# Optimization experiments

Measured on AMD Instinct MI355X. Metric: run time of the kernel, lower is better.

Reference implementation:

```python
import jax, jax.numpy as jnp
import numpy as np

D = 128      # feature dim
H = 8        # heads
DH = D // H  # dim per head
N = 100000   # nodes
E = 600000   # edges
BN_EPS = 1e-5


def _bn(x, g, b, m, v):
    # BatchNorm1d in eval mode (running stats)
    return (x - m) * jax.lax.rsqrt(v + BN_EPS) * g + b


def setup_inputs() -> dict:
    key = jax.random.key(0)
    ks = jax.random.split(key, 32)
    s = 1.0 / np.sqrt(D)
    inp = {
        "x": jax.random.normal(ks[0], (N, D), jnp.float32),
        "edge_index": jax.random.randint(ks[1], (2, E), 0, N, jnp.int64),
        # type embeddings (1 node type, 1 edge type)
        "nt_emb": jax.random.normal(ks[2], (1, D), jnp.float32),
        "et_emb": jax.random.normal(ks[3], (1, D), jnp.float32),
        # merge_node_edge_attr: Linear(2D,D) -> BN -> ReLU -> Linear(D,D)
        "mW1": jax.random.normal(ks[4], (2 * D, D), jnp.float32) * s,
        "mb1": jnp.zeros((D,), jnp.float32),
        "m_g": jnp.ones((D,), jnp.float32),
        "m_b": jnp.zeros((D,), jnp.float32),
        "m_m": jax.random.normal(ks[5], (D,), jnp.float32) * 0.1,
        "m_v": jax.random.uniform(ks[6], (D,), jnp.float32, 0.5, 1.5),
        "mW2": jax.random.normal(ks[7], (D, D), jnp.float32) * s,
        "mb2": jnp.zeros((D,), jnp.float32),
        # residual projection (no bias)
        "resW": jax.random.normal(ks[8], (D, D), jnp.float32) * s,
        # attention projections
        "qW": jax.random.normal(ks[9], (D, D), jnp.float32) * s,
        "qb": jnp.zeros((D,), jnp.float32),
        "kW": jax.random.normal(ks[10], (D, D), jnp.float32) * s,
        "kb": jnp.zeros((D,), jnp.float32),
        "vW": jax.random.normal(ks[11], (D, D), jnp.float32) * s,
        "vb": jnp.zeros((D,), jnp.float32),
        # output mlp: Linear -> BN -> LeakyReLU -> Linear
        "oW1": jax.random.normal(ks[12], (D, D), jnp.float32) * s,
        "ob1": jnp.zeros((D,), jnp.float32),
        "o_g": jnp.ones((D,), jnp.float32),
        "o_b": jnp.zeros((D,), jnp.float32),
        "o_m": jax.random.normal(ks[13], (D,), jnp.float32) * 0.1,
        "o_v": jax.random.uniform(ks[14], (D,), jnp.float32, 0.5, 1.5),
        "oW2": jax.random.normal(ks[15], (D, D), jnp.float32) * s,
        "ob2": jnp.zeros((D,), jnp.float32),
    }
    return inp


def reference(x, edge_index, nt_emb, et_emb, mW1, mb1, m_g, m_b, m_m, m_v, mW2, mb2,
              resW, qW, qb, kW, kb, vW, vb, oW1, ob1, o_g, o_b, o_m, o_v, oW2, ob2):
    src = edge_index[0]
    dst = edge_index[1]
    n_nodes = x.shape[0]
    e = edge_index.shape[1]

    # GraphNodeEdgeAttr: edge attrs are constant per edge type; with one node
    # type, edge_attr[0] == edge_attr[1] == merge(cat[node_emb, edge_emb]).
    merged = jnp.concatenate([nt_emb[0], et_emb[0]])          # [2D]
    h = jax.nn.relu(_bn(merged @ mW1 + mb1, m_g, m_b, m_m, m_v))
    ea = h @ mW2 + mb2                                        # [D], broadcasts per edge

    # edge_update: per-edge multi-head attention scores
    x_j = x[src]                                              # [E, D] source feats
    x_i = x[dst]                                              # [E, D] target feats
    q = ((x_j + ea) @ qW + qb).reshape(e, H, DH) / jnp.sqrt(jnp.float32(DH))
    k = ((x_i + ea) @ kW + kb).reshape(e, H, DH)
    msg = (x_j @ vW + vb).reshape(e, H, DH)
    scores = jnp.sum(q * k, axis=2)                           # [E, H]

    # segment softmax keyed by source node index
    smax = jax.ops.segment_max(scores, src, num_segments=n_nodes)
    ex = jnp.exp(scores - smax[src])
    ssum = jax.ops.segment_sum(ex, src, num_segments=n_nodes)
    alpha = ex / ssum[src]                                    # [E, H]

    # message + scatter-add aggregation to destination nodes
    weighted = (msg * alpha[:, :, None]).reshape(e, H * DH)   # [E, D]
    aggr = jax.ops.segment_sum(weighted, dst, num_segments=n_nodes)  # [N, D]

    res = x @ resW
    z = aggr + res
    out = jax.nn.leaky_relu(_bn(z @ oW1 + ob1, o_g, o_b, o_m, o_v)) @ oW2 + ob2
    return out
```

## Files before the change

kernel.cpp:

```cpp
#include <hip/hip_runtime.h>

#define BN_EPS 1e-5f
#define SCAN_CHUNK 1024
#define BM 128

typedef __attribute__((ext_vector_type(8))) short s16x8;
typedef __attribute__((ext_vector_type(8))) ushort u16x8;
typedef __attribute__((ext_vector_type(4))) float f32x4;

__device__ __forceinline__ ushort f2bf_rne(float f)
{
    unsigned u = __builtin_bit_cast(unsigned, f);
    return (ushort)((u + 0x7fffu + ((u >> 16) & 1u)) >> 16);
}

__device__ __forceinline__ float bf2f(ushort u)
{
    return __builtin_bit_cast(float, (unsigned)u << 16);
}

__global__ __launch_bounds__(128) void k_ea(
    const float* __restrict__ nt, const float* __restrict__ et,
    const float* __restrict__ mW1, const float* __restrict__ mb1,
    const float* __restrict__ m_g, const float* __restrict__ m_b,
    const float* __restrict__ m_m, const float* __restrict__ m_v,
    const float* __restrict__ mW2, const float* __restrict__ mb2,
    const float* __restrict__ qW, const float* __restrict__ qb,
    const float* __restrict__ kW, const float* __restrict__ kb,
    float* __restrict__ eaq, float* __restrict__ eak)
{
    __shared__ float merged[256];
    __shared__ float h[128];
    __shared__ float sea[128];
    const int t = threadIdx.x;
    merged[t]       = nt[t];
    merged[128 + t] = et[t];
    __syncthreads();
    float acc = mb1[t];
    for (int i = 0; i < 256; ++i) acc = fmaf(merged[i], mW1[i * 128 + t], acc);
    acc = (acc - m_m[t]) * rsqrtf(m_v[t] + BN_EPS) * m_g[t] + m_b[t];
    h[t] = acc > 0.f ? acc : 0.f;
    __syncthreads();
    float acc2 = mb2[t];
    for (int k = 0; k < 128; ++k) acc2 = fmaf(h[k], mW2[k * 128 + t], acc2);
    sea[t] = acc2;
    __syncthreads();
    float aq = qb[t], ak = kb[t];
    for (int k = 0; k < 128; ++k) {
        const float e = sea[k];
        aq = fmaf(e, qW[k * 128 + t], aq);
        ak = fmaf(e, kW[k * 128 + t], ak);
    }
    eaq[t] = aq;
    eak[t] = ak;
}

__device__ __forceinline__ void split_store(float w, ushort* __restrict__ base,
                                            int j, int k)
{
    unsigned u = __builtin_bit_cast(unsigned, w);
    unsigned hi = (u + 0x7fffu + ((u >> 16) & 1u)) >> 16;
    float hif = __builtin_bit_cast(float, hi << 16);
    float res = w - hif;
    unsigned lo = __builtin_bit_cast(unsigned, res) >> 16;
    base[j * 128 + k]         = (ushort)hi;
    base[16384 + j * 128 + k] = (ushort)lo;
}

__global__ __launch_bounds__(128) void k_prep3(
    const float* __restrict__ W0, const float* __restrict__ W1,
    const float* __restrict__ W2, ushort* __restrict__ P)
{
    const int j = blockIdx.x;
    const int m = blockIdx.y;
    const int k = threadIdx.x;
    const float* W = (m == 0) ? W0 : (m == 1) ? W1 : W2;
    split_store(W[k * 128 + j], P + (size_t)m * 32768, j, k);
}

__global__ __launch_bounds__(128) void k_prep_out(
    const float* __restrict__ resW, const float* __restrict__ oW1,
    const float* __restrict__ oW2, ushort* __restrict__ P)
{
    __shared__ float col[128];
    const int j = blockIdx.x;
    const int m = blockIdx.y;
    const int k = threadIdx.x;
    float w;
    if (m == 0) {
        col[k] = oW1[k * 128 + j];
        __syncthreads();
        float acc = 0.f;
        for (int i = 0; i < 128; ++i) acc = fmaf(resW[k * 128 + i], col[i], acc);
        w = acc;
    } else {
        const float* W = (m == 1) ? oW1 : oW2;
        w = W[k * 128 + j];
    }
    split_store(w, P + (size_t)m * 32768, j, k);
}

template <int NT>
__device__ __forceinline__ void stage_w(const ushort* __restrict__ wpl,
                                        ushort* __restrict__ sw, int tid)
{
    const uint4* src = (const uint4*)wpl;
#pragma unroll
    for (int it = 0; it < 4096 / NT; ++it) {
        const int idx = it * NT + tid;
        const uint4 v = src[idx];
        const int plane = idx >> 11;
        const int rr = (idx >> 4) & 127;
        const int cb = (idx & 15) << 4;
        const int byteoff = ((rr * 256 + cb) ^ ((rr & 7) << 4));
        *(uint4*)((char*)sw + plane * 32768 + byteoff) = v;
    }
}

template <int NT>
__device__ __forceinline__ void stage_w1(const ushort* __restrict__ wpl,
                                         ushort* __restrict__ sw, int tid)
{
    const uint4* src = (const uint4*)wpl;
#pragma unroll
    for (int it = 0; it < 2048 / NT; ++it) {
        const int idx = it * NT + tid;
        const uint4 v = src[idx];
        const int rr = idx >> 4;
        const int cb = (idx & 15) << 4;
        const int byteoff = ((rr * 256 + cb) ^ ((rr & 7) << 4));
        *(uint4*)((char*)sw + byteoff) = v;
    }
}

__device__ __forceinline__ void split_row(const float* __restrict__ row, int g,
                                          s16x8* ah, s16x8* al)
{
#pragma unroll
    for (int ks = 0; ks < 4; ++ks) {
        const float* ap = row + ks * 32 + g * 8;
        const float4 a0 = *(const float4*)(ap);
        const float4 a1 = *(const float4*)(ap + 4);
        float av[8] = {a0.x, a0.y, a0.z, a0.w, a1.x, a1.y, a1.z, a1.w};
#pragma unroll
        for (int j = 0; j < 8; ++j) {
            const unsigned u = __builtin_bit_cast(unsigned, av[j]);
            ah[ks][j] = (short)(u >> 16);
            const float hif = __builtin_bit_cast(float, u & 0xffff0000u);
            const float res = av[j] - hif;
            al[ks][j] = (short)(__builtin_bit_cast(unsigned, res) >> 16);
        }
    }
}

template <int CT>
__device__ __forceinline__ void mm_core(const float* __restrict__ Arow,
                                        const ushort* __restrict__ sw,
                                        int g, int r16, int ct0, f32x4* acc)
{
#pragma unroll
    for (int ks = 0; ks < 4; ++ks) {
        const float* ap = Arow + ks * 32 + g * 8;
        const float4 a0 = *(const float4*)(ap);
        const float4 a1 = *(const float4*)(ap + 4);
        float av[8] = {a0.x, a0.y, a0.z, a0.w, a1.x, a1.y, a1.z, a1.w};
        s16x8 ahi, alo;
#pragma unroll
        for (int j = 0; j < 8; ++j) {
            const unsigned u = __builtin_bit_cast(unsigned, av[j]);
            ahi[j] = (short)(u >> 16);
            const float hif = __builtin_bit_cast(float, u & 0xffff0000u);
            const float res = av[j] - hif;
            alo[j] = (short)(__builtin_bit_cast(unsigned, res) >> 16);
        }
        const int koff = ks * 64 + g * 16;
#pragma unroll
        for (int ct = 0; ct < CT; ++ct) {
            const int row = (ct0 + ct) * 16 + r16;
            const int byteoff = ((row * 256 + koff) ^ ((row & 7) << 4));
            const s16x8 bhi = *(const s16x8*)((const char*)sw + byteoff);
            const s16x8 blo = *(const s16x8*)((const char*)sw + 32768 + byteoff);
            acc[ct] = __builtin_amdgcn_mfma_f32_16x16x32_bf16(ahi, bhi, acc[ct], 0, 0, 0);
            acc[ct] = __builtin_amdgcn_mfma_f32_16x16x32_bf16(ahi, blo, acc[ct], 0, 0, 0);
            acc[ct] = __builtin_amdgcn_mfma_f32_16x16x32_bf16(alo, bhi, acc[ct], 0, 0, 0);
        }
    }
}

template <int CT>
__device__ __forceinline__ void mm_pass2(const s16x8* ah, const s16x8* al,
                                         const ushort* __restrict__ sw,
                                         int g, int r16, int ct0, f32x4* acc)
{
#pragma unroll
    for (int ks = 0; ks < 4; ++ks) {
        const int koff = ks * 64 + g * 16;
#pragma unroll
        for (int ct = 0; ct < CT; ++ct) {
            const int row = (ct0 + ct) * 16 + r16;
            const int byteoff = ((row * 256 + koff) ^ ((row & 7) << 4));
            const s16x8 b = *(const s16x8*)((const char*)sw + byteoff);
            acc[ct] = __builtin_amdgcn_mfma_f32_16x16x32_bf16(ah[ks], b, acc[ct], 0, 0, 0);
            acc[ct] = __builtin_amdgcn_mfma_f32_16x16x32_bf16(al[ks], b, acc[ct], 0, 0, 0);
        }
    }
}

template <int CT>
__device__ __forceinline__ void mm_pass1(const s16x8* a,
                                         const ushort* __restrict__ sw,
                                         int g, int r16, int ct0, f32x4* acc)
{
#pragma unroll
    for (int ks = 0; ks < 4; ++ks) {
        const int koff = ks * 64 + g * 16;
#pragma unroll
        for (int ct = 0; ct < CT; ++ct) {
            const int row = (ct0 + ct) * 16 + r16;
            const int byteoff = ((row * 256 + koff) ^ ((row & 7) << 4));
            const s16x8 b = *(const s16x8*)((const char*)sw + byteoff);
            acc[ct] = __builtin_amdgcn_mfma_f32_16x16x32_bf16(a[ks], b, acc[ct], 0, 0, 0);
        }
    }
}

__global__ __launch_bounds__(1024, 8) void k_mm_qkv(
    const float* __restrict__ x, const ushort* __restrict__ planes,
    const float* __restrict__ eaq, const float* __restrict__ eak,
    const float* __restrict__ vb,
    ushort* __restrict__ Q16, float* __restrict__ K, ushort* __restrict__ V16, int N)
{
    __shared__ ushort sw[2 * 128 * 128];
    const int tid = threadIdx.x;
    const int sel = blockIdx.y;
    stage_w<1024>(planes + (size_t)sel * 32768, sw, tid);
    __syncthreads();

    const int wave = tid >> 6, lane = tid & 63;
    const int g = lane >> 4, r16 = lane & 15;
    const int wr = wave & 7, wc = wave >> 3;
    const int ct0 = wc * 4;
    const int n0 = blockIdx.x * BM;
    const int arow = wr * 16 + r16;
    int nA = n0 + arow; if (nA >= N) nA = N - 1;

    f32x4 acc[4];
#pragma unroll
    for (int ct = 0; ct < 4; ++ct) acc[ct] = (f32x4){0.f, 0.f, 0.f, 0.f};
    mm_core<4>(x + (size_t)nA * 128, sw, g, r16, ct0, acc);
    __syncthreads();

    if (sel != 1) {
        ushort* vbuf = (ushort*)sw;
        const float* bias  = sel ? vb  : eaq;
        ushort* Obf        = sel ? V16 : Q16;
        const float scale  = sel ? 1.0f : 0.25f;
#pragma unroll
        for (int ct = 0; ct < 4; ++ct) {
            const int c = (ct0 + ct) * 16 + r16;
            const float bc = bias[c];
#pragma unroll
            for (int r = 0; r < 4; ++r) {
                const int nrel = wr * 16 + g * 4 + r;
                vbuf[nrel * 128 + c] = f2bf_rne((acc[ct][r] + bc) * scale);
            }
        }
        __syncthreads();
        const int row = tid >> 3;
        const int col = (tid & 7) * 16;
        if (n0 + row < N) {
            const uint4* src = (const uint4*)(vbuf + row * 128 + col);
            const uint4 v0 = src[0], v1 = src[1];
            uint4* dst = (uint4*)(Obf + (size_t)(n0 + row) * 128 + col);
            dst[0] = v0; dst[1] = v1;
        }
    } else {
        float* fbuf = (float*)sw;
#pragma unroll
        for (int ct = 0; ct < 4; ++ct) {
            const int c = (ct0 + ct) * 16 + r16;
            const float bc = eak[c];
#pragma unroll
            for (int r = 0; r < 4; ++r) {
                const int nrel = wr * 16 + g * 4 + r;
                const int byteoff = (nrel * 512 + c * 4) ^ ((nrel & 7) << 4);
                *(float*)((char*)fbuf + byteoff) = acc[ct][r] + bc;
            }
        }
        __syncthreads();
        const float4* fb4 = (const float4*)fbuf;
#pragma unroll
        for (int it = 0; it < 4; ++it) {
            const int idx4 = it * 1024 + tid;
            const int row = idx4 >> 5;
            const int n = n0 + row;
            if (n < N)
                *(float4*)(K + (size_t)n * 128 + (idx4 & 31) * 4) =
                    fb4[row * 32 + ((idx4 & 31) ^ (row & 7))];
        }
    }
}

__global__ __launch_bounds__(512, 4) void k_out4(
    const float* __restrict__ x, const ushort* __restrict__ Po,
    const float* __restrict__ aggr, const float* __restrict__ ob1,
    const float* __restrict__ o_m, const float* __restrict__ o_v,
    const float* __restrict__ o_g, const float* __restrict__ o_b,
    const float* __restrict__ ob2, float* __restrict__ out, int N)
{
    __shared__ ushort lds[2 * 128 * 128];
    ushort* sw = lds;
    ushort* tb = lds + 16384;
    const int tid = threadIdx.x;
    const int wave = tid >> 6, lane = tid & 63;
    const int g = lane >> 4, r16 = lane & 15;
    const int wr = wave;
    const int n0 = blockIdx.x * 128;
    const int arow = wr * 16 + r16;
    int nA = n0 + arow; if (nA >= N) nA = N - 1;

    s16x8 ah[4], al[4];
    split_row(x + (size_t)nA * 128, g, ah, al);

    f32x4 acc[8];
#pragma unroll
    for (int ct = 0; ct < 8; ++ct) acc[ct] = (f32x4){0.f, 0.f, 0.f, 0.f};

    stage_w1<512>(Po, sw, tid); __syncthreads();
    mm_pass2<8>(ah, al, sw, g, r16, 0, acc); __syncthreads();
    stage_w1<512>(Po + 16384, sw, tid); __syncthreads();
    mm_pass1<8>(ah, sw, g, r16, 0, acc); __syncthreads();

    split_row(aggr + (size_t)nA * 128, g, ah, al);
    stage_w1<512>(Po + 32768, sw, tid); __syncthreads();
    mm_pass2<8>(ah, al, sw, g, r16, 0, acc); __syncthreads();
    stage_w1<512>(Po + 49152, sw, tid); __syncthreads();
    mm_pass1<8>(ah, sw, g, r16, 0, acc); __syncthreads();

#pragma unroll
    for (int ct = 0; ct < 8; ++ct) {
        const int c = ct * 16 + r16;
        const float bc = ob1[c];
        const float rs = rsqrtf(o_v[c] + BN_EPS);
        const float mm = o_m[c], gg = o_g[c], bb = o_b[c];
#pragma unroll
        for (int r = 0; r < 4; ++r) {
            const int nrel = wr * 16 + g * 4 + r;
            float u = acc[ct][r] + bc;
            u = (u - mm) * rs * gg + bb;
            u = u > 0.f ? u : 0.01f * u;
            const int byteoff = ((nrel * 256 + c * 2) ^ ((nrel & 7) << 4));
            *(ushort*)((char*)tb + byteoff) = f2bf_rne(u);
        }
    }
    stage_w1<512>(Po + 65536, sw, tid);
    __syncthreads();

    s16x8 ta[4];
#pragma unroll
    for (int ks = 0; ks < 4; ++ks) {
        const int byteoff = ((arow * 256 + ks * 64 + g * 16) ^ ((arow & 7) << 4));
        ta[ks] = *(const s16x8*)((const char*)tb + byteoff);
    }
#pragma unroll
    for (int ct = 0; ct < 8; ++ct) acc[ct] = (f32x4){0.f, 0.f, 0.f, 0.f};
    mm_pass1<8>(ta, sw, g, r16, 0, acc);
    __syncthreads();
    stage_w1<512>(Po + 81920, sw, tid); __syncthreads();
    mm_pass1<8>(ta, sw, g, r16, 0, acc);
    __syncthreads();

    float* fbuf = (float*)lds;
#pragma unroll
    for (int ct = 0; ct < 8; ++ct) {
        const int c = ct * 16 + r16;
        const float bc = ob2[c];
#pragma unroll
        for (int r = 0; r < 4; ++r) {
            const int nrel = wr * 16 + g * 4 + r;
            const int byteoff = (nrel * 512 + c * 4) ^ ((nrel & 7) << 4);
            *(float*)((char*)fbuf + byteoff) = acc[ct][r] + bc;
        }
    }
    __syncthreads();
    const float4* fb4 = (const float4*)fbuf;
#pragma unroll
    for (int it = 0; it < 8; ++it) {
        const int idx4 = it * 512 + tid;
        const int row = idx4 >> 5;
        const int n = n0 + row;
        if (n < N)
            *(float4*)(out + (size_t)n * 128 + (idx4 & 31) * 4) =
                fb4[row * 32 + ((idx4 & 31) ^ (row & 7))];
    }
}

__global__ __launch_bounds__(256) void k_edge1csr(
    const int* __restrict__ esrc, const int* __restrict__ row_start,
    const int* __restrict__ deg, const ushort* __restrict__ Q16,
    const float* __restrict__ K, float* __restrict__ exp_,
    float* __restrict__ ssum, int N)
{
    const int tid = threadIdx.x;
    const int n = blockIdx.x * 4 + (tid >> 6);
    if (n >= N) return;
    const int lane = tid & 63;
    const int sub = lane >> 4;
    const int l = lane & 15;
    const int h = l >> 1;
    const int c0 = l * 8;
    const int rs = row_start[n];
    const int dg = deg[n];
    const float4 k0 = *(const float4*)(K + (size_t)n * 128 + c0);
    const float4 k1 = *(const float4*)(K + (size_t)n * 128 + c0 + 4);
    for (int j = sub; j < dg; j += 4) {
        const int idx = rs + j;
        const int s = esrc[idx];
        const u16x8 qv = *(const u16x8*)(Q16 + (size_t)s * 128 + c0);
        float p = bf2f(qv[0]) * k0.x + bf2f(qv[1]) * k0.y
                + bf2f(qv[2]) * k0.z + bf2f(qv[3]) * k0.w
                + bf2f(qv[4]) * k1.x + bf2f(qv[5]) * k1.y
                + bf2f(qv[6]) * k1.z + bf2f(qv[7]) * k1.w;
        p += __shfl_xor(p, 1, 64);
        if ((l & 1) == 0) {
            const float v = __expf(p);
            exp_[(size_t)idx * 8 + h] = v;
            unsafeAtomicAdd(&ssum[(size_t)s * 8 + h], v);
        }
    }
}

__global__ __launch_bounds__(256) void k_rsum(float* __restrict__ ssum, int M)
{
    const int i = blockIdx.x * 256 + threadIdx.x;
    if (i < M) ssum[i] = 1.0f / ssum[i];
}

__global__ __launch_bounds__(256) void k_hist(const int* __restrict__ ei,
                                              int* __restrict__ deg, int E)
{
    const int e = blockIdx.x * 256 + threadIdx.x;
    if (e < E) atomicAdd(&deg[ei[E + e]], 1);
}

__global__ __launch_bounds__(256) void k_scan_partial(const int* __restrict__ deg,
                                                      int* __restrict__ part, int N)
{
    __shared__ int sd[256];
    const int b = blockIdx.x, t = threadIdx.x;
    const int base = b * SCAN_CHUNK + t * 4;
    int s = 0;
#pragma unroll
    for (int i = 0; i < 4; ++i) { const int idx = base + i; if (idx < N) s += deg[idx]; }
    sd[t] = s; __syncthreads();
    for (int off = 128; off > 0; off >>= 1) {
        if (t < off) sd[t] += sd[t + off];
        __syncthreads();
    }
    if (t == 0) part[b] = sd[0];
}

__global__ __launch_bounds__(256) void k_scan_top(int* __restrict__ part, int nb)
{
    __shared__ int sd[256];
    const int t = threadIdx.x;
    const int orig = (t < nb) ? part[t] : 0;
    sd[t] = orig;
    __syncthreads();
    for (int off = 1; off < 256; off <<= 1) {
        const int v = (t >= off) ? sd[t - off] : 0;
        __syncthreads();
        sd[t] += v;
        __syncthreads();
    }
    if (t < nb) part[t] = sd[t] - orig;
}

__global__ __launch_bounds__(256) void k_scan_final(const int* __restrict__ deg,
                                                    const int* __restrict__ part,
                                                    int* __restrict__ row_start,
                                                    int* __restrict__ cursor, int N)
{
    __shared__ int ts[256];
    const int b = blockIdx.x, t = threadIdx.x;
    const int base = b * SCAN_CHUNK + t * 4;
    int v[4]; int s = 0;
#pragma unroll
    for (int i = 0; i < 4; ++i) { const int idx = base + i; v[i] = (idx < N) ? deg[idx] : 0; s += v[i]; }
    ts[t] = s; __syncthreads();
    for (int off = 1; off < 256; off <<= 1) {
        const int vv = (t >= off) ? ts[t - off] : 0;
        __syncthreads();
        ts[t] += vv;
        __syncthreads();
    }
    int run = part[b] + ((t > 0) ? ts[t - 1] : 0);
#pragma unroll
    for (int i = 0; i < 4; ++i) {
        const int idx = base + i;
        if (idx < N) { row_start[idx] = run; cursor[idx] = run; run += v[i]; }
    }
}

__global__ __launch_bounds__(256) void k_scatter(const int* __restrict__ ei,
                                                 int* __restrict__ cursor,
                                                 int* __restrict__ esrc, int E)
{
    const int e = blockIdx.x * 256 + threadIdx.x;
    if (e < E) {
        const int pos = atomicAdd(&cursor[ei[E + e]], 1);
        esrc[pos] = ei[e];
    }
}

__global__ __launch_bounds__(256) void k_aggr(
    const int* __restrict__ esrc, const int* __restrict__ row_start,
    const int* __restrict__ deg, const ushort* __restrict__ V16,
    const float* __restrict__ exp_, const float* __restrict__ rsum,
    float* __restrict__ aggr, int N)
{
    const int tid = threadIdx.x;
    const int n = blockIdx.x * 4 + (tid >> 6);
    if (n >= N) return;
    const int lane = tid & 63;
    const int sub = lane >> 4;
    const int l = lane & 15;
    const int h = l >> 1;
    const int c0 = l * 8;
    const int rs = row_start[n];
    const int dg = deg[n];
    float a0 = 0.f, a1 = 0.f, a2 = 0.f, a3 = 0.f;
    float a4 = 0.f, a5 = 0.f, a6 = 0.f, a7 = 0.f;
    for (int j = sub; j < dg; j += 4) {
        const int idx = rs + j;
        const int s = esrc[idx];
        const float a = exp_[(size_t)idx * 8 + h] * rsum[(size_t)s * 8 + h];
        const u16x8 vu = *(const u16x8*)(V16 + (size_t)s * 128 + c0);
        a0 = fmaf(bf2f(vu[0]), a, a0);
        a1 = fmaf(bf2f(vu[1]), a, a1);
        a2 = fmaf(bf2f(vu[2]), a, a2);
        a3 = fmaf(bf2f(vu[3]), a, a3);
        a4 = fmaf(bf2f(vu[4]), a, a4);
        a5 = fmaf(bf2f(vu[5]), a, a5);
        a6 = fmaf(bf2f(vu[6]), a, a6);
        a7 = fmaf(bf2f(vu[7]), a, a7);
    }
    a0 += __shfl_xor(a0, 16, 64); a0 += __shfl_xor(a0, 32, 64);
    a1 += __shfl_xor(a1, 16, 64); a1 += __shfl_xor(a1, 32, 64);
    a2 += __shfl_xor(a2, 16, 64); a2 += __shfl_xor(a2, 32, 64);
    a3 += __shfl_xor(a3, 16, 64); a3 += __shfl_xor(a3, 32, 64);
    a4 += __shfl_xor(a4, 16, 64); a4 += __shfl_xor(a4, 32, 64);
    a5 += __shfl_xor(a5, 16, 64); a5 += __shfl_xor(a5, 32, 64);
    a6 += __shfl_xor(a6, 16, 64); a6 += __shfl_xor(a6, 32, 64);
    a7 += __shfl_xor(a7, 16, 64); a7 += __shfl_xor(a7, 32, 64);
    if (sub == 0) {
        float4 o0 = make_float4(a0, a1, a2, a3);
        float4 o1 = make_float4(a4, a5, a6, a7);
        *(float4*)(aggr + (size_t)n * 128 + c0)     = o0;
        *(float4*)(aggr + (size_t)n * 128 + c0 + 4) = o1;
    }
}

extern "C" void kernel_launch(void* const* d_in, const int* in_sizes, int n_in,
                              void* d_out, int out_size, void* d_ws, size_t ws_size,
                              hipStream_t stream)
{
    const float* x    = (const float*)d_in[0];
    const int*   ei   = (const int*)d_in[1];
    const float* nt   = (const float*)d_in[2];
    const float* et   = (const float*)d_in[3];
    const float* mW1  = (const float*)d_in[4];
    const float* mb1  = (const float*)d_in[5];
    const float* m_g  = (const float*)d_in[6];
    const float* m_b  = (const float*)d_in[7];
    const float* m_m  = (const float*)d_in[8];
    const float* m_v  = (const float*)d_in[9];
    const float* mW2  = (const float*)d_in[10];
    const float* mb2  = (const float*)d_in[11];
    const float* resW = (const float*)d_in[12];
    const float* qW   = (const float*)d_in[13];
    const float* qb   = (const float*)d_in[14];
    const float* kW   = (const float*)d_in[15];
    const float* kb   = (const float*)d_in[16];
    const float* vW   = (const float*)d_in[17];
    const float* vb   = (const float*)d_in[18];
    const float* oW1  = (const float*)d_in[19];
    const float* ob1  = (const float*)d_in[20];
    const float* o_g  = (const float*)d_in[21];
    const float* o_b  = (const float*)d_in[22];
    const float* o_m  = (const float*)d_in[23];
    const float* o_v  = (const float*)d_in[24];
    const float* oW2  = (const float*)d_in[25];
    const float* ob2  = (const float*)d_in[26];
    float* out = (float*)d_out;

    const int N = in_sizes[0] / 128;
    const int E = in_sizes[1] / 2;

    float* ws   = (float*)d_ws;
    float* eaq  = ws;
    float* eak  = ws + 128;
    float* Q    = ws + 256;
    float* K    = Q + (size_t)N * 128;
    float* V    = K + (size_t)N * 128;
    float* exp_ = V + (size_t)N * 128;
    float* ssum = exp_ + (size_t)E * 8;
    int* deg       = (int*)(ssum + (size_t)N * 8);
    int* row_start = deg + N;
    int* cursor    = row_start + N;
    int* part      = cursor + N;
    int* esrc      = part + 256;
    float* aggr = Q;
    ushort* Q16 = (ushort*)Q;
    ushort* V16 = (ushort*)V;
    ushort* Pq = (ushort*)ssum;
    ushort* Po = (ushort*)exp_;

    const int nbm  = (N + BM - 1) / BM;
    const int nbo  = (N + 127) / 128;
    const int nbsc = (N + SCAN_CHUNK - 1) / SCAN_CHUNK;

    k_prep3<<<dim3(128, 3), 128, 0, stream>>>(qW, kW, vW, Pq);
    k_ea<<<1, 128, 0, stream>>>(nt, et, mW1, mb1, m_g, m_b, m_m, m_v, mW2, mb2,
                                qW, qb, kW, kb, eaq, eak);
    k_mm_qkv<<<dim3(nbm, 3), 1024, 0, stream>>>(x, Pq, eaq, eak, vb, Q16, K, V16, N);

    hipMemsetAsync(ssum, 0, (size_t)N * 8 * sizeof(float), stream);
    hipMemsetAsync(deg, 0, (size_t)N * sizeof(int), stream);

    k_hist<<<(E + 255) / 256, 256, 0, stream>>>(ei, deg, E);
    k_scan_partial<<<nbsc, 256, 0, stream>>>(deg, part, N);
    k_scan_top<<<1, 256, 0, stream>>>(part, nbsc);
    k_scan_final<<<nbsc, 256, 0, stream>>>(deg, part, row_start, cursor, N);
    k_scatter<<<(E + 255) / 256, 256, 0, stream>>>(ei, cursor, esrc, E);

    k_edge1csr<<<(N + 3) / 4, 256, 0, stream>>>(esrc, row_start, deg, Q16, K, exp_, ssum, N);
    k_rsum<<<(N * 8 + 255) / 256, 256, 0, stream>>>(ssum, N * 8);
    k_aggr<<<(N + 3) / 4, 256, 0, stream>>>(esrc, row_start, deg, V16, exp_, ssum, aggr, N);

    k_prep_out<<<dim3(128, 3), 128, 0, stream>>>(resW, oW1, oW2, Po);
    k_out4<<<nbo, 512, 0, stream>>>(x, Po, aggr, ob1, o_m, o_v, o_g, o_b, ob2, out, N);
}
```

Before: 435.3 us.

## Store K in bf16 and process 8 edges per wave in edge kernels

K is now written as bf16 like Q and V, which halves its write and read traffic and lets the QKV GEMM use a single epilogue path. The grid order of the QKV GEMM is swapped so the three projections of one row tile run on adjacent blocks, which may improve L2 reuse of x. The score and aggregation kernels now give each lane a full 16-wide head slice and process 8 edges per wave instead of 4. This removes the per-edge shuffle in the score kernel but adds one more reduction shuffle step and more registers per lane in aggregation. K loses precision by being rounded to bf16.

```diff
diff --git a/kernel.cpp b/kernel.cpp
--- a/kernel.cpp
+++ b/kernel.cpp
@@ -228,11 +228,11 @@
     const float* __restrict__ x, const ushort* __restrict__ planes,
     const float* __restrict__ eaq, const float* __restrict__ eak,
     const float* __restrict__ vb,
-    ushort* __restrict__ Q16, float* __restrict__ K, ushort* __restrict__ V16, int N)
+    ushort* __restrict__ Q16, ushort* __restrict__ K16, ushort* __restrict__ V16, int N)
 {
     __shared__ ushort sw[2 * 128 * 128];
     const int tid = threadIdx.x;
-    const int sel = blockIdx.y;
+    const int sel = blockIdx.x;
     stage_w<1024>(planes + (size_t)sel * 32768, sw, tid);
     __syncthreads();
 
@@ -240,7 +240,7 @@
     const int g = lane >> 4, r16 = lane & 15;
     const int wr = wave & 7, wc = wave >> 3;
     const int ct0 = wc * 4;
-    const int n0 = blockIdx.x * BM;
+    const int n0 = blockIdx.y * BM;
     const int arow = wr * 16 + r16;
     int nA = n0 + arow; if (nA >= N) nA = N - 1;
 
@@ -250,54 +250,28 @@
     mm_core<4>(x + (size_t)nA * 128, sw, g, r16, ct0, acc);
     __syncthreads();
 
-    if (sel != 1) {
-        ushort* vbuf = (ushort*)sw;
-        const float* bias  = sel ? vb  : eaq;
-        ushort* Obf        = sel ? V16 : Q16;
-        const float scale  = sel ? 1.0f : 0.25f;
-#pragma unroll
-        for (int ct = 0; ct < 4; ++ct) {
-            const int c = (ct0 + ct) * 16 + r16;
-            const float bc = bias[c];
-#pragma unroll
-            for (int r = 0; r < 4; ++r) {
-                const int nrel = wr * 16 + g * 4 + r;
-                vbuf[nrel * 128 + c] = f2bf_rne((acc[ct][r] + bc) * scale);
-            }
-        }
-        __syncthreads();
-        const int row = tid >> 3;
-        const int col = (tid & 7) * 16;
-        if (n0 + row < N) {
-            const uint4* src = (const uint4*)(vbuf + row * 128 + col);
-            const uint4 v0 = src[0], v1 = src[1];
-            uint4* dst = (uint4*)(Obf + (size_t)(n0 + row) * 128 + col);
-            dst[0] = v0; dst[1] = v1;
-        }
-    } else {
-        float* fbuf = (float*)sw;
-#pragma unroll
-        for (int ct = 0; ct < 4; ++ct) {
-            const int c = (ct0 + ct) * 16 + r16;
-            const float bc = eak[c];
-#pragma unroll
-            for (int r = 0; r < 4; ++r) {
-                const int nrel = wr * 16 + g * 4 + r;
-                const int byteoff = (nrel * 512 + c * 4) ^ ((nrel & 7) << 4);
-                *(float*)((char*)fbuf + byteoff) = acc[ct][r] + bc;
-            }
-        }
-        __syncthreads();
-        const float4* fb4 = (const float4*)fbuf;
-#pragma unroll
-        for (int it = 0; it < 4; ++it) {
-            const int idx4 = it * 1024 + tid;
-            const int row = idx4 >> 5;
-            const int n = n0 + row;
-            if (n < N)
-                *(float4*)(K + (size_t)n * 128 + (idx4 & 31) * 4) =
-                    fb4[row * 32 + ((idx4 & 31) ^ (row & 7))];
-        }
+    ushort* vbuf = (ushort*)sw;
+    const float* bias = (sel == 0) ? eaq : (sel == 1) ? eak : vb;
+    ushort* Obf       = (sel == 0) ? Q16 : (sel == 1) ? K16 : V16;
+    const float scale = (sel == 0) ? 0.25f : 1.0f;
+#pragma unroll
+    for (int ct = 0; ct < 4; ++ct) {
+        const int c = (ct0 + ct) * 16 + r16;
+        const float bc = bias[c];
+#pragma unroll
+        for (int r = 0; r < 4; ++r) {
+            const int nrel = wr * 16 + g * 4 + r;
+            vbuf[nrel * 128 + c] = f2bf_rne((acc[ct][r] + bc) * scale);
+        }
+    }
+    __syncthreads();
+    const int row = tid >> 3;
+    const int col = (tid & 7) * 16;
+    if (n0 + row < N) {
+        const uint4* src = (const uint4*)(vbuf + row * 128 + col);
+        const uint4 v0 = src[0], v1 = src[1];
+        uint4* dst = (uint4*)(Obf + (size_t)(n0 + row) * 128 + col);
+        dst[0] = v0; dst[1] = v1;
     }
 }
 
@@ -398,35 +372,37 @@
 __global__ __launch_bounds__(256) void k_edge1csr(
     const int* __restrict__ esrc, const int* __restrict__ row_start,
     const int* __restrict__ deg, const ushort* __restrict__ Q16,
-    const float* __restrict__ K, float* __restrict__ exp_,
+    const ushort* __restrict__ K16, float* __restrict__ exp_,
     float* __restrict__ ssum, int N)
 {
     const int tid = threadIdx.x;
     const int n = blockIdx.x * 4 + (tid >> 6);
     if (n >= N) return;
     const int lane = tid & 63;
-    const int sub = lane >> 4;
-    const int l = lane & 15;
-    const int h = l >> 1;
-    const int c0 = l * 8;
+    const int sub = lane >> 3;
+    const int h = lane & 7;
+    const int c0 = h * 16;
     const int rs = row_start[n];
     const int dg = deg[n];
-    const float4 k0 = *(const float4*)(K + (size_t)n * 128 + c0);
-    const float4 k1 = *(const float4*)(K + (size_t)n * 128 + c0 + 4);
-    for (int j = sub; j < dg; j += 4) {
+    const u16x8 ka = *(const u16x8*)(K16 + (size_t)n * 128 + c0);
+    const u16x8 kb = *(const u16x8*)(K16 + (size_t)n * 128 + c0 + 8);
+    float kr[16];
+#pragma unroll
+    for (int i = 0; i < 8; ++i) { kr[i] = bf2f(ka[i]); kr[8 + i] = bf2f(kb[i]); }
+    for (int j = sub; j < dg; j += 8) {
         const int idx = rs + j;
         const int s = esrc[idx];
-        const u16x8 qv = *(const u16x8*)(Q16 + (size_t)s * 128 + c0);
-        float p = bf2f(qv[0]) * k0.x + bf2f(qv[1]) * k0.y
-                + bf2f(qv[2]) * k0.z + bf2f(qv[3]) * k0.w
-                + bf2f(qv[4]) * k1.x + bf2f(qv[5]) * k1.y
-                + bf2f(qv[6]) * k1.z + bf2f(qv[7]) * k1.w;
-        p += __shfl_xor(p, 1, 64);
-        if ((l & 1) == 0) {
-            const float v = __expf(p);
-            exp_[(size_t)idx * 8 + h] = v;
-            unsafeAtomicAdd(&ssum[(size_t)s * 8 + h], v);
-        }
+        const u16x8 qa = *(const u16x8*)(Q16 + (size_t)s * 128 + c0);
+        const u16x8 qb_ = *(const u16x8*)(Q16 + (size_t)s * 128 + c0 + 8);
+        float p = 0.f;
+#pragma unroll
+        for (int i = 0; i < 8; ++i) {
+            p = fmaf(bf2f(qa[i]),  kr[i],     p);
+            p = fmaf(bf2f(qb_[i]), kr[8 + i], p);
+        }
+        const float v = __expf(p);
+        exp_[(size_t)idx * 8 + h] = v;
+        unsafeAtomicAdd(&ssum[(size_t)s * 8 + h], v);
     }
 }
 
@@ -523,41 +499,39 @@
     const int n = blockIdx.x * 4 + (tid >> 6);
     if (n >= N) return;
     const int lane = tid & 63;
-    const int sub = lane >> 4;
-    const int l = lane & 15;
-    const int h = l >> 1;
-    const int c0 = l * 8;
+    const int sub = lane >> 3;
+    const int h = lane & 7;
+    const int c0 = h * 16;
     const int rs = row_start[n];
     const int dg = deg[n];
-    float a0 = 0.f, a1 = 0.f, a2 = 0.f, a3 = 0.f;
-    float a4 = 0.f, a5 = 0.f, a6 = 0.f, a7 = 0.f;
-    for (int j = sub; j < dg; j += 4) {
+    float acc[16];
+#pragma unroll
+    for (int i = 0; i < 16; ++i) acc[i] = 0.f;
+    for (int j = sub; j < dg; j += 8) {
         const int idx = rs + j;
         const int s = esrc[idx];
         const float a = exp_[(size_t)idx * 8 + h] * rsum[(size_t)s * 8 + h];
-        const u16x8 vu = *(const u16x8*)(V16 + (size_t)s * 128 + c0);
-        a0 = fmaf(bf2f(vu[0]), a, a0);
-        a1 = fmaf(bf2f(vu[1]), a, a1);
-        a2 = fmaf(bf2f(vu[2]), a, a2);
-        a3 = fmaf(bf2f(vu[3]), a, a3);
-        a4 = fmaf(bf2f(vu[4]), a, a4);
-        a5 = fmaf(bf2f(vu[5]), a, a5);
-        a6 = fmaf(bf2f(vu[6]), a, a6);
-        a7 = fmaf(bf2f(vu[7]), a, a7);
-    }
-    a0 += __shfl_xor(a0, 16, 64); a0 += __shfl_xor(a0, 32, 64);
-    a1 += __shfl_xor(a1, 16, 64); a1 += __shfl_xor(a1, 32, 64);
-    a2 += __shfl_xor(a2, 16, 64); a2 += __shfl_xor(a2, 32, 64);
-    a3 += __shfl_xor(a3, 16, 64); a3 += __shfl_xor(a3, 32, 64);
-    a4 += __shfl_xor(a4, 16, 64); a4 += __shfl_xor(a4, 32, 64);
-    a5 += __shfl_xor(a5, 16, 64); a5 += __shfl_xor(a5, 32, 64);
-    a6 += __shfl_xor(a6, 16, 64); a6 += __shfl_xor(a6, 32, 64);
-    a7 += __shfl_xor(a7, 16, 64); a7 += __shfl_xor(a7, 32, 64);
+        const u16x8 v0 = *(const u16x8*)(V16 + (size_t)s * 128 + c0);
+        const u16x8 v1 = *(const u16x8*)(V16 + (size_t)s * 128 + c0 + 8);
+#pragma unroll
+        for (int i = 0; i < 8; ++i) {
+            acc[i]     = fmaf(bf2f(v0[i]), a, acc[i]);
+            acc[8 + i] = fmaf(bf2f(v1[i]), a, acc[8 + i]);
+        }
+    }
+#pragma unroll
+    for (int i = 0; i < 16; ++i) {
+        acc[i] += __shfl_xor(acc[i], 8, 64);
+        acc[i] += __shfl_xor(acc[i], 16, 64);
+        acc[i] += __shfl_xor(acc[i], 32, 64);
+    }
     if (sub == 0) {
-        float4 o0 = make_float4(a0, a1, a2, a3);
-        float4 o1 = make_float4(a4, a5, a6, a7);
-        *(float4*)(aggr + (size_t)n * 128 + c0)     = o0;
-        *(float4*)(aggr + (size_t)n * 128 + c0 + 4) = o1;
+#pragma unroll
+        for (int q = 0; q < 4; ++q) {
+            float4 o = make_float4(acc[q * 4], acc[q * 4 + 1],
+                                   acc[q * 4 + 2], acc[q * 4 + 3]);
+            *(float4*)(aggr + (size_t)n * 128 + c0 + q * 4) = o;
+        }
     }
 }
 
@@ -612,6 +586,7 @@
     int* esrc      = part + 256;
     float* aggr = Q;
     ushort* Q16 = (ushort*)Q;
+    ushort* K16 = (ushort*)K;
     ushort* V16 = (ushort*)V;
     ushort* Pq = (ushort*)ssum;
     ushort* Po = (ushort*)exp_;
@@ -623,7 +598,7 @@
     k_prep3<<<dim3(128, 3), 128, 0, stream>>>(qW, kW, vW, Pq);
     k_ea<<<1, 128, 0, stream>>>(nt, et, mW1, mb1, m_g, m_b, m_m, m_v, mW2, mb2,
                                 qW, qb, kW, kb, eaq, eak);
-    k_mm_qkv<<<dim3(nbm, 3), 1024, 0, stream>>>(x, Pq, eaq, eak, vb, Q16, K, V16, N);
+    k_mm_qkv<<<dim3(3, nbm), 1024, 0, stream>>>(x, Pq, eaq, eak, vb, Q16, K16, V16, N);
 
     hipMemsetAsync(ssum, 0, (size_t)N * 8 * sizeof(float), stream);
     hipMemsetAsync(deg, 0, (size_t)N * sizeof(int), stream);
@@ -634,7 +609,7 @@
     k_scan_final<<<nbsc, 256, 0, stream>>>(deg, part, row_start, cursor, N);
     k_scatter<<<(E + 255) / 256, 256, 0, stream>>>(ei, cursor, esrc, E);
 
-    k_edge1csr<<<(N + 3) / 4, 256, 0, stream>>>(esrc, row_start, deg, Q16, K, exp_, ssum, N);
+    k_edge1csr<<<(N + 3) / 4, 256, 0, stream>>>(esrc, row_start, deg, Q16, K16, exp_, ssum, N);
     k_rsum<<<(N * 8 + 255) / 256, 256, 0, stream>>>(ssum, N * 8);
     k_aggr<<<(N + 3) / 4, 256, 0, stream>>>(esrc, row_start, deg, V16, exp_, ssum, aggr, N);
 
```

Measured after the change: 437.9 us. No clear change (+0.6%).
